# Optimization experiments

Hardware: AMD Instinct MI355X
Metric: run time of the kernel (lower is better)

Reference implementation:

```python
import jax, jax.numpy as jnp
import numpy as np

N_NODES = 100000
N_EDGES = 1600000
IN_CH, HID_CH, OUT_CH = 128, 64, 64


def setup_inputs() -> dict:
    key = jax.random.key(0)
    ks = jax.random.split(key, 6)
    x = jax.random.normal(ks[0], (N_NODES, IN_CH), dtype=jnp.float32)
    edge_index = jax.random.randint(ks[1], (2, N_EDGES), 0, N_NODES, dtype=jnp.int64)
    W1 = jax.random.normal(ks[2], (IN_CH, HID_CH), dtype=jnp.float32) / np.float32(np.sqrt(IN_CH))
    b1 = jax.random.normal(ks[3], (HID_CH,), dtype=jnp.float32) * 0.01
    W2 = jax.random.normal(ks[4], (HID_CH, OUT_CH), dtype=jnp.float32) / np.float32(np.sqrt(HID_CH))
    b2 = jax.random.normal(ks[5], (OUT_CH,), dtype=jnp.float32) * 0.01
    return {"x": x, "edge_index": edge_index, "W1": W1, "b1": b1, "W2": W2, "b2": b2}


def gcn_conv(x, W, b, src, dst, n_nodes):
    """PyG GCNConv: h = x@W; add self-loops; sym-normalized scatter-add; + bias."""
    h = x @ W  # (N, F_out)
    # degree on graph WITH self-loops (unit edge weights): deg[i] = in-degree + 1
    deg = jax.ops.segment_sum(jnp.ones((src.shape[0],), h.dtype), dst, num_segments=n_nodes) + 1.0
    dinv = jax.lax.rsqrt(deg)  # deg >= 1, no div-by-zero
    norm = dinv[src] * dinv[dst]  # (E,)
    msg = h[src] * norm[:, None]  # (E, F_out) gather + scale
    agg = jax.ops.segment_sum(msg, dst, num_segments=n_nodes)  # scatter-add
    agg = agg + h * (dinv * dinv)[:, None]  # self-loop contribution deg^-1 * h_i
    return agg + b


def reference(x, edge_index, W1, b1, W2, b2):
    src, dst = edge_index[0], edge_index[1]  # source_to_target flow
    n = x.shape[0]
    h = jax.nn.relu(gcn_conv(x, W1, b1, src, dst, n))
    out = gcn_conv(h, W2, b2, src, dst, n)
    return out
```

## Files before the change

kernel.cpp:

```cpp
#include <hip/hip_runtime.h>
#include <hip/hip_fp16.h>


#define CHUNK 2048
#define BCAP  8192
#define NB_PAD 512
#define BSHIFT 8
#define BMASK 255

typedef _Float16 f16x8 __attribute__((ext_vector_type(8)));
typedef float f32x4 __attribute__((ext_vector_type(4)));

__device__ __forceinline__ unsigned int pack2(float a, float b) {
  __half2 h = __floats2half2_rn(a, b);
  return *reinterpret_cast<unsigned int*>(&h);
}
__device__ __forceinline__ __half2 h2add(__half2 a, __half2 b) {
  return __hadd2(a, b);
}
__device__ __forceinline__ __half2 bcast_h2(unsigned int u) {
  return *reinterpret_cast<__half2*>(&u);
}

__global__ __launch_bounds__(256) void initcur_kernel(int* __restrict__ bcursor,
                                                      int nb) {
  int i = blockIdx.x * 256 + threadIdx.x;
  if (i < nb) bcursor[i] = i * BCAP;
}

__global__ __launch_bounds__(512) void chunksort_kernel(
    const int* __restrict__ src, const int* __restrict__ dst,
    int* __restrict__ bcursor, int* __restrict__ ebuck, int nE, int nb) {
  __shared__ int hist[NB_PAD];
  __shared__ int loff[NB_PAD];
  __shared__ int gbase[NB_PAD];
  __shared__ int lcur[NB_PAD];
  __shared__ int wsum[8];
  __shared__ int srec[CHUNK];
  __shared__ int saddr[CHUNK];
  const int t = threadIdx.x;
  const int lane = t & 63, w = t >> 6;
  const int e0 = blockIdx.x * CHUNK;
  const int n = min(CHUNK, nE - e0);
  hist[t] = 0;
  __syncthreads();
  for (int i = t; i < n; i += 512) atomicAdd(&hist[dst[e0 + i] >> BSHIFT], 1);
  __syncthreads();
  int h = hist[t];
  int x = h;
#pragma unroll
  for (int off = 1; off < 64; off <<= 1) {
    int v = __shfl_up(x, off);
    if (lane >= off) x += v;
  }
  if (lane == 63) wsum[w] = x;
  __syncthreads();
  if (w == 0 && lane < 8) {
    int s = wsum[lane];
#pragma unroll
    for (int off = 1; off < 8; off <<= 1) {
      int v = __shfl_up(s, off);
      if (lane >= off) s += v;
    }
    wsum[lane] = s;
  }
  __syncthreads();
  int excl = ((w == 0) ? 0 : wsum[w - 1]) + x - h;
  loff[t] = excl;
  lcur[t] = excl;
  if (t < nb) gbase[t] = h ? atomicAdd(&bcursor[t], h) : 0;
  __syncthreads();
  for (int i = t; i < n; i += 512) {
    int d = dst[e0 + i];
    int b = d >> BSHIFT;
    int p = atomicAdd(&lcur[b], 1);
    srec[p] = src[e0 + i] | ((d & BMASK) << 17);
    saddr[p] = gbase[b] + (p - loff[b]);
  }
  __syncthreads();
  for (int i = t; i < n; i += 512) ebuck[saddr[i]] = srec[i];
}

__global__ __launch_bounds__(1024) void bucketsort_kernel(
    const int* __restrict__ ebuck, const int* __restrict__ bcursor,
    int* __restrict__ esrc, int* __restrict__ rowptr,
    float* __restrict__ dinv, int N, int E, int nb) {
  __shared__ int hist[256];
  __shared__ int rowcur[256];
  __shared__ int red[1024];
  __shared__ int wsum[4];
  __shared__ int gbs;
  const int t = threadIdx.x;
  const int bk = blockIdx.x;
  const int base = bk * BCAP;
  const int cnt = bcursor[bk] - base;
  int partial = 0;
  for (int j = t; j < bk; j += 1024) partial += bcursor[j] - j * BCAP;
  red[t] = partial;
  if (t < 256) hist[t] = 0;
  __syncthreads();
  for (int off = 512; off > 0; off >>= 1) {
    if (t < off) red[t] += red[t + off];
    __syncthreads();
  }
  if (t == 0) gbs = red[0];
  for (int i = t; i < cnt; i += 1024)
    atomicAdd(&hist[(ebuck[base + i] >> 17) & BMASK], 1);
  __syncthreads();
  const int gb = gbs;
  int h = 0, x = 0;
  const int lane = t & 63, w = t >> 6;
  if (t < 256) {
    h = hist[t];
    x = h;
#pragma unroll
    for (int off = 1; off < 64; off <<= 1) {
      int v = __shfl_up(x, off);
      if (lane >= off) x += v;
    }
    if (lane == 63) wsum[w] = x;
  }
  __syncthreads();
  if (t == 0) {
    int run = 0;
#pragma unroll
    for (int j = 0; j < 4; ++j) {
      int v = wsum[j];
      wsum[j] = run;
      run += v;
    }
  }
  __syncthreads();
  if (t < 256) {
    int excl = wsum[w] + x - h;
    rowcur[t] = excl;
    int node = bk * 256 + t;
    if (node < N) {
      rowptr[node] = gb + excl;
      dinv[node] = rsqrtf((float)h + 1.0f);
    }
  }
  if (bk == nb - 1 && t == 0) rowptr[N] = E;
  __syncthreads();
  for (int i = t; i < cnt; i += 1024) {
    int rec = ebuck[base + i];
    int p = atomicAdd(&rowcur[(rec >> 17) & BMASK], 1);
    esrc[gb + p] = rec & 0x1FFFF;
  }
}

template <int K, bool IN_HALF>
__global__ __launch_bounds__(256) void gemm_mfma(const void* __restrict__ Xin,
                                                 const float* __restrict__ W,
                                                 const float* __restrict__ dinv,
                                                 __half* __restrict__ H, int N) {
  __shared__ __align__(16) unsigned char sA[128 * K * 2];
  __shared__ __align__(16) unsigned char sB[64 * K * 2];
  const int t = threadIdx.x;
  const int brow = blockIdx.x * 128;
  constexpr int CH = K / 8;
  for (int idx = t; idx < 128 * CH; idx += 256) {
    int r = idx / CH, c = idx - r * CH;
    int row = brow + r;
    if (row >= N) row = N - 1;
    unsigned int off = (unsigned int)((r * K + c * 8) * 2) ^ ((r & 7) << 4);
    uint4 pk;
    if constexpr (IN_HALF) {
      pk = *reinterpret_cast<const uint4*>((const __half*)Xin + (size_t)row * K + c * 8);
    } else {
      const float4* xp =
          reinterpret_cast<const float4*>((const float*)Xin + (size_t)row * K + c * 8);
      float4 f0 = xp[0], f1 = xp[1];
      pk.x = pack2(f0.x, f0.y);
      pk.y = pack2(f0.z, f0.w);
      pk.z = pack2(f1.x, f1.y);
      pk.w = pack2(f1.z, f1.w);
    }
    *reinterpret_cast<uint4*>(sA + off) = pk;
  }
  for (int idx = t; idx < K * 64; idx += 256) {
    int k = idx >> 6, n = idx & 63;
    __half h = __float2half_rn(W[idx]);
    unsigned int off = (unsigned int)((n * K + k) * 2) ^ ((n & 7) << 4);
    *reinterpret_cast<unsigned short*>(sB + off) =
        *reinterpret_cast<unsigned short*>(&h);
  }
  __syncthreads();

  const int wv = t >> 6, l = t & 63;
  const int lr = l & 15;
  const int lk = (l >> 4) * 8;
  f32x4 acc[2][4] = {};
#pragma unroll
  for (int ks = 0; ks < K / 32; ++ks) {
    f16x8 af[2], bf[4];
#pragma unroll
    for (int m = 0; m < 2; ++m) {
      int r = wv * 32 + m * 16 + lr;
      unsigned int off = (unsigned int)((r * K + ks * 32 + lk) * 2) ^ ((r & 7) << 4);
      af[m] = *reinterpret_cast<const f16x8*>(sA + off);
    }
#pragma unroll
    for (int n = 0; n < 4; ++n) {
      int cc = n * 16 + lr;
      unsigned int off = (unsigned int)((cc * K + ks * 32 + lk) * 2) ^ ((cc & 7) << 4);
      bf[n] = *reinterpret_cast<const f16x8*>(sB + off);
    }
#pragma unroll
    for (int m = 0; m < 2; ++m)
#pragma unroll
      for (int n = 0; n < 4; ++n)
        acc[m][n] = __builtin_amdgcn_mfma_f32_16x16x32_f16(af[m], bf[n], acc[m][n],
                                                           0, 0, 0);
  }
#pragma unroll
  for (int m = 0; m < 2; ++m) {
#pragma unroll
    for (int j = 0; j < 4; ++j) {
      int row = brow + wv * 32 + m * 16 + (l >> 4) * 4 + j;
      if (row < N) {
        float di = dinv[row];
#pragma unroll
        for (int n = 0; n < 4; ++n) {
          float v = acc[m][n][j] * di;
          H[(size_t)row * 64 + n * 16 + lr] = __float2half_rn(v);
        }
      }
    }
  }
}

__global__ __launch_bounds__(256) void agg_gemm_kernel(
    const __half* __restrict__ hs, const int* __restrict__ rowptr,
    const int* __restrict__ esrc, const float* __restrict__ dinv,
    const float* __restrict__ b, const float* __restrict__ W2,
    __half* __restrict__ H2, int N) {
  __shared__ __align__(16) unsigned char sY[16 * 64 * 2];
  __shared__ __align__(16) unsigned char sW[64 * 64 * 2];
  const int t = threadIdx.x;
  for (int idx = t; idx < 64 * 64; idx += 256) {
    int k = idx >> 6, n = idx & 63;
    __half h = __float2half_rn(W2[idx]);
    unsigned int off = (unsigned int)((n * 64 + k) * 2) ^ ((n & 7) << 4);
    *reinterpret_cast<unsigned short*>(sW + off) =
        *reinterpret_cast<unsigned short*>(&h);
  }

  const int wv = t >> 6;
  const int lane = t & 63;
  const int nid = lane >> 4;
  const int g = (lane >> 3) & 1;
  const int cl = lane & 7;
  const int nodeL = wv * 4 + nid;
  const int node = blockIdx.x * 16 + nodeL;
  const unsigned int choff = (unsigned int)cl << 4;
  const unsigned char* __restrict__ hb = (const unsigned char*)hs;
  int beg = 0, end = 0;
  if (node < N) {
    beg = rowptr[node];
    end = rowptr[node + 1];
  }
  __half2 accA[4] = {{0.f, 0.f}, {0.f, 0.f}, {0.f, 0.f}, {0.f, 0.f}};
  __half2 accB[4] = {{0.f, 0.f}, {0.f, 0.f}, {0.f, 0.f}, {0.f, 0.f}};
  int k = beg + g;
  while (k < end) {
    int s0 = esrc[min(k,     end - 1)];
    int s1 = esrc[min(k + 2, end - 1)];
    int s2 = esrc[min(k + 4, end - 1)];
    int s3 = esrc[min(k + 6, end - 1)];
    uint4 v0 = *reinterpret_cast<const uint4*>(hb + (((unsigned int)s0 << 7) + choff));
    uint4 v1 = *reinterpret_cast<const uint4*>(hb + (((unsigned int)s1 << 7) + choff));
    uint4 v2 = *reinterpret_cast<const uint4*>(hb + (((unsigned int)s2 << 7) + choff));
    uint4 v3 = *reinterpret_cast<const uint4*>(hb + (((unsigned int)s3 << 7) + choff));
    {
      accA[0] = h2add(accA[0], bcast_h2(v0.x));
      accA[1] = h2add(accA[1], bcast_h2(v0.y));
      accA[2] = h2add(accA[2], bcast_h2(v0.z));
      accA[3] = h2add(accA[3], bcast_h2(v0.w));
    }
    if (k + 2 < end) {
      accB[0] = h2add(accB[0], bcast_h2(v1.x));
      accB[1] = h2add(accB[1], bcast_h2(v1.y));
      accB[2] = h2add(accB[2], bcast_h2(v1.z));
      accB[3] = h2add(accB[3], bcast_h2(v1.w));
    }
    if (k + 4 < end) {
      accA[0] = h2add(accA[0], bcast_h2(v2.x));
      accA[1] = h2add(accA[1], bcast_h2(v2.y));
      accA[2] = h2add(accA[2], bcast_h2(v2.z));
      accA[3] = h2add(accA[3], bcast_h2(v2.w));
    }
    if (k + 6 < end) {
      accB[0] = h2add(accB[0], bcast_h2(v3.x));
      accB[1] = h2add(accB[1], bcast_h2(v3.y));
      accB[2] = h2add(accB[2], bcast_h2(v3.z));
      accB[3] = h2add(accB[3], bcast_h2(v3.w));
    }
    k += 8;
  }
#pragma unroll
  for (int r = 0; r < 4; ++r) accA[r] = h2add(accA[r], accB[r]);
#pragma unroll
  for (int r = 0; r < 4; ++r) {
    int u = __shfl_xor(*reinterpret_cast<int*>(&accA[r]), 8);
    accA[r] = h2add(accA[r], *reinterpret_cast<__half2*>(&u));
  }
  if (g == 0 && node < N) {
    uint4 sv = *reinterpret_cast<const uint4*>(hb + (((unsigned int)node << 7) + choff));
    float di = dinv[node];
    const float4* bv = reinterpret_cast<const float4*>(b);
    float4 b0 = bv[cl * 2], b1 = bv[cl * 2 + 1];
    float r[8];
#pragma unroll
    for (int q = 0; q < 4; ++q) {
      float2 av = __half22float2(accA[q]);
      float2 sf = __half22float2(bcast_h2((&sv.x)[q]));
      r[2 * q]     = (av.x + sf.x) * di;
      r[2 * q + 1] = (av.y + sf.y) * di;
    }
    r[0] += b0.x; r[1] += b0.y; r[2] += b0.z; r[3] += b0.w;
    r[4] += b1.x; r[5] += b1.y; r[6] += b1.z; r[7] += b1.w;
#pragma unroll
    for (int q = 0; q < 8; ++q) r[q] = fmaxf(r[q], 0.f);
    uint4 pk;
    pk.x = pack2(r[0], r[1]);
    pk.y = pack2(r[2], r[3]);
    pk.z = pack2(r[4], r[5]);
    pk.w = pack2(r[6], r[7]);
    unsigned int off = (unsigned int)((nodeL * 64 + cl * 8) * 2) ^ ((nodeL & 7) << 4);
    *reinterpret_cast<uint4*>(sY + off) = pk;
  }
  __syncthreads();
  if (wv == 0) {
    const int lr = lane & 15;
    const int lk = (lane >> 4) * 8;
    f32x4 acc[4] = {};
#pragma unroll
    for (int ks = 0; ks < 2; ++ks) {
      unsigned int aoff = (unsigned int)((lr * 64 + ks * 32 + lk) * 2) ^ ((lr & 7) << 4);
      f16x8 af = *reinterpret_cast<const f16x8*>(sY + aoff);
#pragma unroll
      for (int n = 0; n < 4; ++n) {
        int cc = n * 16 + lr;
        unsigned int boff = (unsigned int)((cc * 64 + ks * 32 + lk) * 2) ^ ((cc & 7) << 4);
        f16x8 bf = *reinterpret_cast<const f16x8*>(sW + boff);
        acc[n] = __builtin_amdgcn_mfma_f32_16x16x32_f16(af, bf, acc[n], 0, 0, 0);
      }
    }
#pragma unroll
    for (int j = 0; j < 4; ++j) {
      int rowL = (lane >> 4) * 4 + j;
      int row = blockIdx.x * 16 + rowL;
      if (row < N) {
        float di = dinv[row];
#pragma unroll
        for (int n = 0; n < 4; ++n) {
          float v = acc[n][j] * di;
          H2[(size_t)row * 64 + n * 16 + lr] = __float2half_rn(v);
        }
      }
    }
  }
}

__global__ __launch_bounds__(256) void agg_kernel(const __half* __restrict__ hs,
                                                  const int* __restrict__ rowptr,
                                                  const int* __restrict__ esrc,
                                                  const float* __restrict__ dinv,
                                                  const float* __restrict__ b,
                                                  float* __restrict__ outv, int N) {
  const int wv = threadIdx.x >> 6;
  const int lane = threadIdx.x & 63;
  const int nid = lane >> 4;
  const int g = (lane >> 3) & 1;
  const int cl = lane & 7;
  const int node = blockIdx.x * 16 + wv * 4 + nid;
  const unsigned int choff = (unsigned int)cl << 4;
  const unsigned char* __restrict__ hb = (const unsigned char*)hs;
  int beg = 0, end = 0;
  if (node < N) {
    beg = rowptr[node];
    end = rowptr[node + 1];
  }
  __half2 accA[4] = {{0.f, 0.f}, {0.f, 0.f}, {0.f, 0.f}, {0.f, 0.f}};
  __half2 accB[4] = {{0.f, 0.f}, {0.f, 0.f}, {0.f, 0.f}, {0.f, 0.f}};
  int k = beg + g;
  while (k < end) {
    int s0 = esrc[min(k,     end - 1)];
    int s1 = esrc[min(k + 2, end - 1)];
    int s2 = esrc[min(k + 4, end - 1)];
    int s3 = esrc[min(k + 6, end - 1)];
    uint4 v0 = *reinterpret_cast<const uint4*>(hb + (((unsigned int)s0 << 7) + choff));
    uint4 v1 = *reinterpret_cast<const uint4*>(hb + (((unsigned int)s1 << 7) + choff));
    uint4 v2 = *reinterpret_cast<const uint4*>(hb + (((unsigned int)s2 << 7) + choff));
    uint4 v3 = *reinterpret_cast<const uint4*>(hb + (((unsigned int)s3 << 7) + choff));
    {
      accA[0] = h2add(accA[0], bcast_h2(v0.x));
      accA[1] = h2add(accA[1], bcast_h2(v0.y));
      accA[2] = h2add(accA[2], bcast_h2(v0.z));
      accA[3] = h2add(accA[3], bcast_h2(v0.w));
    }
    if (k + 2 < end) {
      accB[0] = h2add(accB[0], bcast_h2(v1.x));
      accB[1] = h2add(accB[1], bcast_h2(v1.y));
      accB[2] = h2add(accB[2], bcast_h2(v1.z));
      accB[3] = h2add(accB[3], bcast_h2(v1.w));
    }
    if (k + 4 < end) {
      accA[0] = h2add(accA[0], bcast_h2(v2.x));
      accA[1] = h2add(accA[1], bcast_h2(v2.y));
      accA[2] = h2add(accA[2], bcast_h2(v2.z));
      accA[3] = h2add(accA[3], bcast_h2(v2.w));
    }
    if (k + 6 < end) {
      accB[0] = h2add(accB[0], bcast_h2(v3.x));
      accB[1] = h2add(accB[1], bcast_h2(v3.y));
      accB[2] = h2add(accB[2], bcast_h2(v3.z));
      accB[3] = h2add(accB[3], bcast_h2(v3.w));
    }
    k += 8;
  }
#pragma unroll
  for (int r = 0; r < 4; ++r) accA[r] = h2add(accA[r], accB[r]);
#pragma unroll
  for (int r = 0; r < 4; ++r) {
    int u = __shfl_xor(*reinterpret_cast<int*>(&accA[r]), 8);
    accA[r] = h2add(accA[r], *reinterpret_cast<__half2*>(&u));
  }
  if (g == 0 && node < N) {
    uint4 sv = *reinterpret_cast<const uint4*>(hb + (((unsigned int)node << 7) + choff));
    float di = dinv[node];
    const float4* bv = reinterpret_cast<const float4*>(b);
    float4 b0 = bv[cl * 2], b1 = bv[cl * 2 + 1];
    float r[8];
#pragma unroll
    for (int q = 0; q < 4; ++q) {
      float2 av = __half22float2(accA[q]);
      float2 sf = __half22float2(bcast_h2((&sv.x)[q]));
      r[2 * q]     = (av.x + sf.x) * di;
      r[2 * q + 1] = (av.y + sf.y) * di;
    }
    r[0] += b0.x; r[1] += b0.y; r[2] += b0.z; r[3] += b0.w;
    r[4] += b1.x; r[5] += b1.y; r[6] += b1.z; r[7] += b1.w;
    float4* ov = reinterpret_cast<float4*>(outv);
    ov[(size_t)node * 16 + cl * 2]     = make_float4(r[0], r[1], r[2], r[3]);
    ov[(size_t)node * 16 + cl * 2 + 1] = make_float4(r[4], r[5], r[6], r[7]);
  }
}

extern "C" void kernel_launch(void* const* d_in, const int* in_sizes, int n_in,
                              void* d_out, int out_size, void* d_ws, size_t ws_size,
                              hipStream_t stream) {
  const float* x  = (const float*)d_in[0];
  const int*   ei = (const int*)d_in[1];
  const float* W1 = (const float*)d_in[2];
  const float* b1 = (const float*)d_in[3];
  const float* W2 = (const float*)d_in[4];
  const float* b2 = (const float*)d_in[5];
  const int N = in_sizes[0] / 128;
  const int E = in_sizes[1] / 2;
  const int* src = ei;
  const int* dst = ei + E;
  const int nb = (N + 255) >> BSHIFT;

  char* ws = (char*)d_ws;
  int*    bcursor = (int*)ws;
  float*  dinv    = (float*)(ws + (1 << 20));
  int*    rowptr  = (int*)(ws + 3 * (1 << 19));
  int*    esrc    = (int*)(ws + (1 << 21));
  int*    ebuck   = (int*)(ws + 9 * (1 << 20));
  __half* hs      = (__half*)(ws + 22 * (1 << 20));
  __half* hs2     = (__half*)(ws + 36 * (1 << 20));
  float*  out = (float*)d_out;

  initcur_kernel<<<(nb + 255) / 256, 256, 0, stream>>>(bcursor, nb);
  chunksort_kernel<<<(E + CHUNK - 1) / CHUNK, 512, 0, stream>>>(src, dst, bcursor,
                                                                ebuck, E, nb);
  bucketsort_kernel<<<nb, 1024, 0, stream>>>(ebuck, bcursor, esrc, rowptr,
                                             dinv, N, E, nb);

  const int gemmGrid = (N + 127) / 128;
  const int aggGrid = (N + 15) / 16;
  gemm_mfma<128, false><<<gemmGrid, 256, 0, stream>>>(x, W1, dinv, hs, N);
  agg_gemm_kernel<<<aggGrid, 256, 0, stream>>>(hs, rowptr, esrc, dinv, b1, W2,
                                               hs2, N);
  agg_kernel<<<aggGrid, 256, 0, stream>>>(hs2, rowptr, esrc, dinv, b2, out, N);
}
```

Baseline: 130.8 us.

## Simplify chunk bucketing to scatter directly to global without LDS staging

The chunk-sort kernel no longer computes a local prefix scan or stages records in shared memory before writing. Each edge now takes a per-bucket slot from a shared-memory atomic counter and writes straight to its global bucket position. Chunk size doubles and the block grows to 1024 threads, which halves the number of global bucket-cursor atomics. The cost is less coalesced global writes, since consecutive edges in a bucket come from threads in arbitrary order.

```diff
diff --git a/kernel.cpp b/kernel.cpp
--- a/kernel.cpp
+++ b/kernel.cpp
@@ -2,7 +2,7 @@
 #include <hip/hip_fp16.h>
 
 
-#define CHUNK 2048
+#define CHUNK 4096
 #define BCAP  8192
 #define NB_PAD 512
 #define BSHIFT 8
@@ -28,57 +28,31 @@
   if (i < nb) bcursor[i] = i * BCAP;
 }
 
-__global__ __launch_bounds__(512) void chunksort_kernel(
+__global__ __launch_bounds__(1024) void chunksort_kernel(
     const int* __restrict__ src, const int* __restrict__ dst,
     int* __restrict__ bcursor, int* __restrict__ ebuck, int nE, int nb) {
   __shared__ int hist[NB_PAD];
-  __shared__ int loff[NB_PAD];
   __shared__ int gbase[NB_PAD];
   __shared__ int lcur[NB_PAD];
-  __shared__ int wsum[8];
-  __shared__ int srec[CHUNK];
-  __shared__ int saddr[CHUNK];
   const int t = threadIdx.x;
-  const int lane = t & 63, w = t >> 6;
   const int e0 = blockIdx.x * CHUNK;
   const int n = min(CHUNK, nE - e0);
-  hist[t] = 0;
-  __syncthreads();
-  for (int i = t; i < n; i += 512) atomicAdd(&hist[dst[e0 + i] >> BSHIFT], 1);
-  __syncthreads();
-  int h = hist[t];
-  int x = h;
-#pragma unroll
-  for (int off = 1; off < 64; off <<= 1) {
-    int v = __shfl_up(x, off);
-    if (lane >= off) x += v;
-  }
-  if (lane == 63) wsum[w] = x;
-  __syncthreads();
-  if (w == 0 && lane < 8) {
-    int s = wsum[lane];
-#pragma unroll
-    for (int off = 1; off < 8; off <<= 1) {
-      int v = __shfl_up(s, off);
-      if (lane >= off) s += v;
-    }
-    wsum[lane] = s;
-  }
-  __syncthreads();
-  int excl = ((w == 0) ? 0 : wsum[w - 1]) + x - h;
-  loff[t] = excl;
-  lcur[t] = excl;
-  if (t < nb) gbase[t] = h ? atomicAdd(&bcursor[t], h) : 0;
-  __syncthreads();
-  for (int i = t; i < n; i += 512) {
+  if (t < NB_PAD) hist[t] = 0;
+  __syncthreads();
+  for (int i = t; i < n; i += 1024) atomicAdd(&hist[dst[e0 + i] >> BSHIFT], 1);
+  __syncthreads();
+  if (t < NB_PAD) {
+    int c = hist[t];
+    gbase[t] = c ? atomicAdd(&bcursor[t], c) : 0;
+    lcur[t] = 0;
+  }
+  __syncthreads();
+  for (int i = t; i < n; i += 1024) {
     int d = dst[e0 + i];
     int b = d >> BSHIFT;
     int p = atomicAdd(&lcur[b], 1);
-    srec[p] = src[e0 + i] | ((d & BMASK) << 17);
-    saddr[p] = gbase[b] + (p - loff[b]);
-  }
-  __syncthreads();
-  for (int i = t; i < n; i += 512) ebuck[saddr[i]] = srec[i];
+    ebuck[gbase[b] + p] = src[e0 + i] | ((d & BMASK) << 17);
+  }
 }
 
 __global__ __launch_bounds__(1024) void bucketsort_kernel(
@@ -474,8 +448,8 @@
   float*  out = (float*)d_out;
 
   initcur_kernel<<<(nb + 255) / 256, 256, 0, stream>>>(bcursor, nb);
-  chunksort_kernel<<<(E + CHUNK - 1) / CHUNK, 512, 0, stream>>>(src, dst, bcursor,
-                                                                ebuck, E, nb);
+  chunksort_kernel<<<(E + CHUNK - 1) / CHUNK, 1024, 0, stream>>>(src, dst, bcursor,
+                                                                 ebuck, E, nb);
   bucketsort_kernel<<<nb, 1024, 0, stream>>>(ebuck, bcursor, esrc, rowptr,
                                              dinv, N, E, nb);
 
```

New measurement: 127.3 us. -2.7%, faster.
